# Kernel optimization log

Hardware: AMD Instinct MI355X
Metric: run time of the kernel (lower is better)

Reference implementation:

```python
import jax, jax.numpy as jnp
import numpy as np

T, K, N = 4096, 4096, 11008  # tokens, in_features, out_features


def _unpack_int4(packed):
    """packed: int8 [..., K//2] -> signed 4-bit values int8 [..., K].
    Low nibble first, high nibble second; arithmetic shifts sign-extend."""
    lo = jnp.right_shift(jnp.left_shift(packed, 4).astype(jnp.int8), 4)
    hi = jnp.right_shift(packed, 4).astype(jnp.int8)
    out = jnp.stack([lo, hi], axis=-1)  # [..., K//2, 2]
    return out.reshape(*packed.shape[:-1], packed.shape[-1] * 2)


def _pack_int4(vals):
    """vals: int8 in [-8,7], [..., K] -> packed int8 [..., K//2]."""
    v = vals.reshape(*vals.shape[:-1], vals.shape[-1] // 2, 2)
    lo = v[..., 0] & 0xF
    hi = v[..., 1] & 0xF
    return (lo | jnp.left_shift(hi, 4)).astype(jnp.int8)


def setup_inputs() -> dict:
    key = jax.random.key(0)
    k1, k2, k3, k4 = jax.random.split(key, 4)
    # symmetric 4-bit quantized values in [-7, 7], packed two per byte
    x_int = jax.random.randint(k1, (T, K), -7, 8).astype(jnp.int8)
    w_int = jax.random.randint(k2, (N, K), -7, 8).astype(jnp.int8)
    pq_x = _pack_int4(x_int)
    weight = _pack_int4(w_int)
    # per-token / per-output-channel dequant scales (max_abs/7 style magnitudes)
    scales_x = (jax.random.uniform(k3, (T,), jnp.float32) * 0.01 + 1e-4)
    weight_scales = (jax.random.uniform(k4, (N,), jnp.float32) * 0.01 + 1e-4)
    return {"pq_x": pq_x, "scales_x": scales_x, "weight": weight,
            "weight_scales": weight_scales}


def reference(pq_x, scales_x, weight, weight_scales):
    # Unpack int4 operands. Products |a*w| <= 49 and K=4096 => |acc| <= 2e5,
    # exactly representable in fp32, so the fp32 matmul equals int32 GEMM.
    a = _unpack_int4(pq_x).astype(jnp.float32)      # [T, K]
    w = _unpack_int4(weight).astype(jnp.float32)    # [N, K]
    acc = jnp.einsum('tk,nk->tn', a, w)             # integer GEMM in fp32
    # fused per-token x per-output-channel dequant
    out = acc * scales_x[:, None] * weight_scales[None, :]
    out = out.astype(jnp.float16)
    return out[None]  # unsqueeze(0) as in the torch module
```

## Files before the change

### kernel.cpp

```cpp
#include <hip/hip_runtime.h>
#include <hip/hip_fp16.h>
#include <stdint.h>


#define T_DIM 4096
#define K_DIM 4096
#define N_DIM 11008
#define KP    2048
#define BM 128
#define BN 128
#define BK 64
#define STAGES 64
#define A_PANELS (T_DIM / BM)
#define B_PANELS (N_DIM / BN)
#define CHUNK 8192
#define WS_A ((size_t)A_PANELS * STAGES * CHUNK)
#define WS_B ((size_t)B_PANELS * STAGES * CHUNK)
#define NA_BYTES ((size_t)T_DIM * KP)
#define NW_BYTES ((size_t)N_DIM * KP)

typedef __attribute__((ext_vector_type(4)))  int int32x4;
typedef __attribute__((ext_vector_type(16))) int int32x16;
typedef __attribute__((ext_vector_type(4)))  float floatx4;
typedef __attribute__((ext_vector_type(8)))  _Float16 f16x8;
typedef __attribute__((ext_vector_type(2)))  _Float16 f16x2;

__device__ __forceinline__ uint32_t pack4(int4 v) {
  return (uint32_t)(v.x & 0xFF) | ((uint32_t)(v.y & 0xFF) << 8) |
         ((uint32_t)(v.z & 0xFF) << 16) | ((uint32_t)(v.w & 0xFF) << 24);
}
__device__ __forceinline__ uint32_t nib_lo_s8(uint32_t p) {
  uint32_t t = (p & 0x0F0F0F0Fu) ^ 0x88888888u;
  return (t - 0x08080808u) ^ 0x80808080u;
}
__device__ __forceinline__ uint32_t nib_hi_s8(uint32_t p) {
  uint32_t t = ((p >> 4) & 0x0F0F0F0Fu) ^ 0x88888888u;
  return (t - 0x08080808u) ^ 0x80808080u;
}

__global__ __launch_bounds__(256) void unpack_tiles(
    const int* __restrict__ xa, const int* __restrict__ xw,
    uint8_t* __restrict__ wsa, uint8_t* __restrict__ wsb)
{
  const int row = blockIdx.x;
  const int g = threadIdx.x;
  const int s = g >> 2, c = g & 3;
  const int* src; uint8_t* dst; int r;
  if (row < T_DIM) {
    src = xa + (size_t)row * KP;
    r = row & (BM - 1);
    dst = wsa + ((size_t)((row >> 7) * STAGES + s)) * CHUNK;
  } else {
    const int rw = row - T_DIM;
    src = xw + (size_t)rw * KP;
    r = rw & (BN - 1);
    dst = wsb + ((size_t)((rw >> 7) * STAGES + s)) * CHUNK;
  }
  const int4* s4 = (const int4*)(src + g * 8);
  const int4 v0 = s4[0], v1 = s4[1];
  const uint32_t b0 = pack4(v0), b1 = pack4(v1);
  uint4 o;
  o.x = nib_lo_s8(b0); o.y = nib_hi_s8(b0);
  o.z = nib_lo_s8(b1); o.w = nib_hi_s8(b1);
  *(uint4*)(dst + c * 2048 + r * 16) = o;
}

__device__ __forceinline__ void dma16(const uint8_t* g, uint8_t* l) {
  __builtin_amdgcn_global_load_lds(
      (const __attribute__((address_space(1))) uint32_t*)g,
      (__attribute__((address_space(3))) uint32_t*)l, 16, 0, 0);
}

__global__ __launch_bounds__(256) void gemm_i8(
    const uint8_t* __restrict__ wsa, const uint8_t* __restrict__ wsb,
    const float* __restrict__ sx, const float* __restrict__ sw,
    float* __restrict__ out)
{
  __shared__ uint8_t sA[CHUNK];
  __shared__ uint8_t sB[CHUNK];

  const int tid  = threadIdx.x;
  const int lane = tid & 63;
  const int wv   = tid >> 6;
  const int wm   = wv >> 1, wn = wv & 1;
  const int h    = lane >> 5;
  const int ml   = lane & 31;
  const int p    = blockIdx.x;
  const int q    = blockIdx.y;

  const uint8_t* chunkA = wsa + (size_t)p * STAGES * CHUNK;
  const uint8_t* chunkB = wsb + (size_t)q * STAGES * CHUNK;
  const int seg = wv * 2048 + lane * 16;
  uint8_t* ldsA0 = &sA[wv * 2048];
  uint8_t* ldsB0 = &sB[wv * 2048];

  const int rowA = (wm * 64 + ml) * 16;
  const int rowB = (wn * 64 + ml) * 16;

  int32x16 acc00, acc01, acc10, acc11;
#pragma unroll
  for (int i = 0; i < 16; ++i) { acc00[i] = 0; acc01[i] = 0; acc10[i] = 0; acc11[i] = 0; }

  dma16(chunkA + seg, ldsA0);
  dma16(chunkA + seg + 1024, ldsA0 + 1024);
  dma16(chunkB + seg, ldsB0);
  dma16(chunkB + seg + 1024, ldsB0 + 1024);

#pragma unroll 1
  for (int s = 0; s < STAGES; ++s) {
    __syncthreads();
#pragma unroll
    for (int s2 = 0; s2 < 2; ++s2) {
      const uint8_t* pa = &sA[(2 * s2 + h) * 2048 + rowA];
      const uint8_t* pb = &sB[(2 * s2 + h) * 2048 + rowB];
      const int32x4 a0 = *(const int32x4*)pa;
      const int32x4 a1 = *(const int32x4*)(pa + 512);
      const int32x4 b0 = *(const int32x4*)pb;
      const int32x4 b1 = *(const int32x4*)(pb + 512);
      acc00 = __builtin_amdgcn_mfma_i32_32x32x32_i8(a0, b0, acc00, 0, 0, 0);
      acc01 = __builtin_amdgcn_mfma_i32_32x32x32_i8(a0, b1, acc01, 0, 0, 0);
      acc10 = __builtin_amdgcn_mfma_i32_32x32x32_i8(a1, b0, acc10, 0, 0, 0);
      acc11 = __builtin_amdgcn_mfma_i32_32x32x32_i8(a1, b1, acc11, 0, 0, 0);
    }
    __syncthreads();
    if (s + 1 < STAGES) {
      const uint8_t* ca = chunkA + (size_t)(s + 1) * CHUNK + seg;
      const uint8_t* cb = chunkB + (size_t)(s + 1) * CHUNK + seg;
      dma16(ca, ldsA0);
      dma16(ca + 1024, ldsA0 + 1024);
      dma16(cb, ldsB0);
      dma16(cb + 1024, ldsB0 + 1024);
    }
  }

#pragma unroll
  for (int mi = 0; mi < 2; ++mi) {
    const int rb = p * BM + wm * 64 + mi * 32 + 4 * h;
#pragma unroll
    for (int ni = 0; ni < 2; ++ni) {
      const int gcol = q * BN + wn * 64 + ni * 32 + ml;
      const float swv = sw[gcol];
      const int32x16 a = (mi == 0) ? (ni == 0 ? acc00 : acc01)
                                   : (ni == 0 ? acc10 : acc11);
#pragma unroll
      for (int r = 0; r < 16; ++r) {
        const int grow = rb + (r & 3) + 8 * (r >> 2);
        const float v = (float)a[r] * sx[grow] * swv;
        out[(size_t)grow * N_DIM + gcol] = __half2float(__float2half(v));
      }
    }
  }
}

__global__ __launch_bounds__(256) void repack_int32_to_bytes(
    const int* __restrict__ xa, const int* __restrict__ xw,
    uint32_t* __restrict__ da, uint32_t* __restrict__ dw)
{
  const size_t i = (size_t)blockIdx.x * blockDim.x + threadIdx.x;
  const size_t na4 = NA_BYTES / 4;
  const int4* src; uint32_t* dst; size_t off;
  if (i < na4) { src = (const int4*)xa; dst = da; off = i; }
  else         { src = (const int4*)xw; dst = dw; off = i - na4; }
  const int4 v = src[off];
  dst[off] = pack4(v);
}

__device__ __forceinline__ uint32_t cvt2(uint32_t m) {
  union U { uint32_t u; f16x2 h; } a, b, c;
  a.u = m ^ 0x64086408u; b.u = 0xE408E408u; c.h = a.h + b.h;
  return c.u;
}
__device__ __forceinline__ void unpack_cell(uint32_t* cell, uint32_t p) {
  cell[0] = cvt2( p        & 0x000F000Fu);
  cell[1] = cvt2((p >> 4)  & 0x000F000Fu);
  cell[2] = cvt2((p >> 8)  & 0x000F000Fu);
  cell[3] = cvt2((p >> 12) & 0x000F000Fu);
}

template <bool PACKED>
__global__ __launch_bounds__(256) void linear4bit_f16(
    const uint8_t* __restrict__ pqx, const float* __restrict__ sx,
    const uint8_t* __restrict__ wq,  const float* __restrict__ sw,
    const int* __restrict__ pqx32,   const int* __restrict__ wq32,
    float* __restrict__ out)
{
  __shared__ uint32_t sAf[8][BM][4];
  __shared__ uint32_t sBf[8][BN][4];
  const int tid = threadIdx.x, lane = tid & 63, wv = tid >> 6;
  const int wm = wv >> 1, wn = wv & 1, qd = lane >> 4, m16 = lane & 15;
  const int bm0 = blockIdx.x * BM, bn0 = blockIdx.y * BN;
  const int srow = tid >> 1, sh = tid & 1;
  const uint8_t* aPtr = pqx + (size_t)(bm0 + srow) * KP + sh * 16;
  const uint8_t* bPtr = wq  + (size_t)(bn0 + srow) * KP + sh * 16;
  const int* aPtr32 = pqx32 + (size_t)(bm0 + srow) * KP + sh * 16;
  const int* bPtr32 = wq32  + (size_t)(bn0 + srow) * KP + sh * 16;
  floatx4 acc[4][4];
#pragma unroll
  for (int mi = 0; mi < 4; ++mi)
#pragma unroll
    for (int ni = 0; ni < 4; ++ni)
#pragma unroll
      for (int r = 0; r < 4; ++r) acc[mi][ni][r] = 0.0f;
  uint4 ar, br;
  auto load_stage = [&](int s) {
    if (PACKED) {
      ar = *(const uint4*)(aPtr + (size_t)s * 32);
      br = *(const uint4*)(bPtr + (size_t)s * 32);
    } else {
      const int4* a4 = (const int4*)(aPtr32 + (size_t)s * 32);
      const int4* b4 = (const int4*)(bPtr32 + (size_t)s * 32);
      ar.x = pack4(a4[0]); ar.y = pack4(a4[1]); ar.z = pack4(a4[2]); ar.w = pack4(a4[3]);
      br.x = pack4(b4[0]); br.y = pack4(b4[1]); br.z = pack4(b4[2]); br.w = pack4(b4[3]);
    }
  };
  auto stage_to_lds = [&]() {
    uint32_t pa[4] = {ar.x, ar.y, ar.z, ar.w};
    uint32_t pb[4] = {br.x, br.y, br.z, br.w};
#pragma unroll
    for (int i = 0; i < 4; ++i) {
      unpack_cell(&sAf[4 * sh + i][srow][0], pa[i]);
      unpack_cell(&sBf[4 * sh + i][srow][0], pb[i]);
    }
  };
  load_stage(0); stage_to_lds();
#pragma unroll 1
  for (int s = 0; s < STAGES; ++s) {
    __syncthreads();
    if (s + 1 < STAGES) load_stage(s + 1);
#pragma unroll
    for (int s2 = 0; s2 < 2; ++s2) {
      f16x8 aF[4], bF[4];
#pragma unroll
      for (int mi = 0; mi < 4; ++mi)
        aF[mi] = *(const f16x8*)&sAf[4 * s2 + qd][wm * 64 + mi * 16 + m16][0];
#pragma unroll
      for (int ni = 0; ni < 4; ++ni)
        bF[ni] = *(const f16x8*)&sBf[4 * s2 + qd][wn * 64 + ni * 16 + m16][0];
#pragma unroll
      for (int mi = 0; mi < 4; ++mi)
#pragma unroll
        for (int ni = 0; ni < 4; ++ni)
          acc[mi][ni] = __builtin_amdgcn_mfma_f32_16x16x32_f16(aF[mi], bF[ni], acc[mi][ni], 0, 0, 0);
    }
    __syncthreads();
    if (s + 1 < STAGES) stage_to_lds();
  }
#pragma unroll
  for (int mi = 0; mi < 4; ++mi) {
    const int grow0 = bm0 + wm * 64 + mi * 16 + qd * 4;
    const float s0 = sx[grow0], s1 = sx[grow0 + 1], s2v = sx[grow0 + 2], s3 = sx[grow0 + 3];
#pragma unroll
    for (int ni = 0; ni < 4; ++ni) {
      const int gcol = bn0 + wn * 64 + ni * 16 + m16;
      const float swv = sw[gcol];
      const floatx4 a = acc[mi][ni];
      out[(size_t)(grow0 + 0) * N_DIM + gcol] = __half2float(__float2half(a[0] * s0 * swv));
      out[(size_t)(grow0 + 1) * N_DIM + gcol] = __half2float(__float2half(a[1] * s1 * swv));
      out[(size_t)(grow0 + 2) * N_DIM + gcol] = __half2float(__float2half(a[2] * s2v * swv));
      out[(size_t)(grow0 + 3) * N_DIM + gcol] = __half2float(__float2half(a[3] * s3 * swv));
    }
  }
}

extern "C" void kernel_launch(void* const* d_in, const int* in_sizes, int n_in,
                              void* d_out, int out_size, void* d_ws, size_t ws_size,
                              hipStream_t stream) {
  const int*   pqx32 = (const int*)d_in[0];
  const float* sxp   = (const float*)d_in[1];
  const int*   wq32  = (const int*)d_in[2];
  const float* swp   = (const float*)d_in[3];
  float* outp = (float*)d_out;

  if (ws_size >= WS_A + WS_B) {
    uint8_t* wsa = (uint8_t*)d_ws;
    uint8_t* wsb = wsa + WS_A;
    unpack_tiles<<<T_DIM + N_DIM, 256, 0, stream>>>(pqx32, wq32, wsa, wsb);
    gemm_i8<<<dim3(A_PANELS, B_PANELS), 256, 0, stream>>>(wsa, wsb, sxp, swp, outp);
  } else if (ws_size >= NA_BYTES + NW_BYTES) {
    uint8_t* da = (uint8_t*)d_ws;
    uint8_t* dw = da + NA_BYTES;
    const size_t total4 = (NA_BYTES + NW_BYTES) / 4;
    repack_int32_to_bytes<<<(uint32_t)(total4 / 256), 256, 0, stream>>>(
        pqx32, wq32, (uint32_t*)da, (uint32_t*)dw);
    linear4bit_f16<true><<<dim3(T_DIM / BM, N_DIM / BN), 256, 0, stream>>>(
        da, sxp, dw, swp, nullptr, nullptr, outp);
  } else {
    linear4bit_f16<false><<<dim3(T_DIM / BM, N_DIM / BN), 256, 0, stream>>>(
        nullptr, sxp, nullptr, swp, pqx32, wq32, outp);
  }
}
```

Before: 492.6 us.

## Widen int8 GEMM tile to 128x256 with double-buffered LDS prefetch

The N tile of the pre-unpacked int8 MFMA GEMM grows from 128 to 256, so each wave computes 2x4 32x32 MFMA tiles, raising reuse of each A fragment. LDS is double-buffered and the next stage's global-to-LDS DMA is issued right after a single barrier, overlapping it with the current stage's MFMAs. The unpack kernel is reorganised to write the new 256-row B chunk layout, and per-row activation scales are hoisted in the epilogue. The cost is more accumulator registers (128 VGPRs of accumulators) and 48KB of LDS per block, which may limit occupancy despite the launch-bounds hint.

```diff
diff --git a/kernel.cpp b/kernel.cpp
--- a/kernel.cpp
+++ b/kernel.cpp
@@ -8,14 +8,14 @@
 #define N_DIM 11008
 #define KP    2048
 #define BM 128
-#define BN 128
-#define BK 64
+#define BN 256
 #define STAGES 64
 #define A_PANELS (T_DIM / BM)
 #define B_PANELS (N_DIM / BN)
-#define CHUNK 8192
-#define WS_A ((size_t)A_PANELS * STAGES * CHUNK)
-#define WS_B ((size_t)B_PANELS * STAGES * CHUNK)
+#define CHUNK_A 8192
+#define CHUNK_B 16384
+#define WS_A ((size_t)A_PANELS * STAGES * CHUNK_A)
+#define WS_B ((size_t)B_PANELS * STAGES * CHUNK_B)
 #define NA_BYTES ((size_t)T_DIM * KP)
 #define NW_BYTES ((size_t)N_DIM * KP)
 
@@ -38,31 +38,39 @@
   return (t - 0x08080808u) ^ 0x80808080u;
 }
 
-__global__ __launch_bounds__(256) void unpack_tiles(
+__global__ __launch_bounds__(256) void unpack_tiles2(
     const int* __restrict__ xa, const int* __restrict__ xw,
     uint8_t* __restrict__ wsa, uint8_t* __restrict__ wsb)
 {
-  const int row = blockIdx.x;
-  const int g = threadIdx.x;
-  const int s = g >> 2, c = g & 3;
-  const int* src; uint8_t* dst; int r;
-  if (row < T_DIM) {
-    src = xa + (size_t)row * KP;
-    r = row & (BM - 1);
-    dst = wsa + ((size_t)((row >> 7) * STAGES + s)) * CHUNK;
+  const int s  = blockIdx.x;
+  const int yb = blockIdx.y;
+  const int t  = threadIdx.x;
+  const int r  = t >> 1, h = t & 1;
+
+  const int* src; uint8_t* dst; int cellStride;
+  if (yb < A_PANELS) {
+    src = xa + ((size_t)(yb * 128 + r)) * KP + s * 32 + h * 16;
+    dst = wsa + ((size_t)yb * STAGES + s) * CHUNK_A + r * 16;
+    cellStride = 2048;
   } else {
-    const int rw = row - T_DIM;
-    src = xw + (size_t)rw * KP;
-    r = rw & (BN - 1);
-    dst = wsb + ((size_t)((rw >> 7) * STAGES + s)) * CHUNK;
-  }
-  const int4* s4 = (const int4*)(src + g * 8);
-  const int4 v0 = s4[0], v1 = s4[1];
+    const int yb2 = yb - A_PANELS;
+    const int panel = yb2 >> 1;
+    const int rip = (yb2 & 1) * 128 + r;
+    src = xw + ((size_t)(yb2 * 128 + r)) * KP + s * 32 + h * 16;
+    dst = wsb + ((size_t)panel * STAGES + s) * CHUNK_B + rip * 16;
+    cellStride = 4096;
+  }
+  const int4* s4 = (const int4*)src;
+  const int4 v0 = s4[0], v1 = s4[1], v2 = s4[2], v3 = s4[3];
   const uint32_t b0 = pack4(v0), b1 = pack4(v1);
-  uint4 o;
-  o.x = nib_lo_s8(b0); o.y = nib_hi_s8(b0);
-  o.z = nib_lo_s8(b1); o.w = nib_hi_s8(b1);
-  *(uint4*)(dst + c * 2048 + r * 16) = o;
+  const uint32_t b2 = pack4(v2), b3 = pack4(v3);
+  uint4 o01, o23;
+  o01.x = nib_lo_s8(b0); o01.y = nib_hi_s8(b0);
+  o01.z = nib_lo_s8(b1); o01.w = nib_hi_s8(b1);
+  o23.x = nib_lo_s8(b2); o23.y = nib_hi_s8(b2);
+  o23.z = nib_lo_s8(b3); o23.w = nib_hi_s8(b3);
+  *(uint4*)(dst + (2 * h    ) * cellStride) = o01;
+  *(uint4*)(dst + (2 * h + 1) * cellStride) = o23;
 }
 
 __device__ __forceinline__ void dma16(const uint8_t* g, uint8_t* l) {
@@ -71,13 +79,13 @@
       (__attribute__((address_space(3))) uint32_t*)l, 16, 0, 0);
 }
 
-__global__ __launch_bounds__(256) void gemm_i8(
+__global__ __launch_bounds__(256, 2) void gemm_i8_db(
     const uint8_t* __restrict__ wsa, const uint8_t* __restrict__ wsb,
     const float* __restrict__ sx, const float* __restrict__ sw,
     float* __restrict__ out)
 {
-  __shared__ uint8_t sA[CHUNK];
-  __shared__ uint8_t sB[CHUNK];
+  __shared__ uint8_t sA[2][CHUNK_A];
+  __shared__ uint8_t sB[2][CHUNK_B];
 
   const int tid  = threadIdx.x;
   const int lane = tid & 63;
@@ -85,67 +93,76 @@
   const int wm   = wv >> 1, wn = wv & 1;
   const int h    = lane >> 5;
   const int ml   = lane & 31;
-  const int p    = blockIdx.x;
-  const int q    = blockIdx.y;
-
-  const uint8_t* chunkA = wsa + (size_t)p * STAGES * CHUNK;
-  const uint8_t* chunkB = wsb + (size_t)q * STAGES * CHUNK;
-  const int seg = wv * 2048 + lane * 16;
-  uint8_t* ldsA0 = &sA[wv * 2048];
-  uint8_t* ldsB0 = &sB[wv * 2048];
+  const int pp   = blockIdx.x;
+  const int qq   = blockIdx.y;
+
+  const uint8_t* chunkA = wsa + (size_t)pp * STAGES * CHUNK_A;
+  const uint8_t* chunkB = wsb + (size_t)qq * STAGES * CHUNK_B;
+  const int segOff = wv * 1024 + lane * 16;
+  const int ldsOff = wv * 1024;
 
   const int rowA = (wm * 64 + ml) * 16;
-  const int rowB = (wn * 64 + ml) * 16;
-
-  int32x16 acc00, acc01, acc10, acc11;
-#pragma unroll
-  for (int i = 0; i < 16; ++i) { acc00[i] = 0; acc01[i] = 0; acc10[i] = 0; acc11[i] = 0; }
-
-  dma16(chunkA + seg, ldsA0);
-  dma16(chunkA + seg + 1024, ldsA0 + 1024);
-  dma16(chunkB + seg, ldsB0);
-  dma16(chunkB + seg + 1024, ldsB0 + 1024);
+  const int rowB = (wn * 128 + ml) * 16;
+
+  int32x16 acc[2][4];
+#pragma unroll
+  for (int mi = 0; mi < 2; ++mi)
+#pragma unroll
+    for (int ni = 0; ni < 4; ++ni)
+#pragma unroll
+      for (int i = 0; i < 16; ++i) acc[mi][ni][i] = 0;
+
+  auto dma_stage = [&](int s, int buf) {
+    const uint8_t* ca = chunkA + (size_t)s * CHUNK_A;
+    const uint8_t* cb = chunkB + (size_t)s * CHUNK_B;
+#pragma unroll
+    for (int i = 0; i < 2; ++i)
+      dma16(ca + segOff + i * 4096, &sA[buf][ldsOff + i * 4096]);
+#pragma unroll
+    for (int i = 0; i < 4; ++i)
+      dma16(cb + segOff + i * 4096, &sB[buf][ldsOff + i * 4096]);
+  };
+
+  dma_stage(0, 0);
 
 #pragma unroll 1
   for (int s = 0; s < STAGES; ++s) {
+    const int buf = s & 1;
     __syncthreads();
+    if (s + 1 < STAGES) dma_stage(s + 1, buf ^ 1);
 #pragma unroll
     for (int s2 = 0; s2 < 2; ++s2) {
-      const uint8_t* pa = &sA[(2 * s2 + h) * 2048 + rowA];
-      const uint8_t* pb = &sB[(2 * s2 + h) * 2048 + rowB];
-      const int32x4 a0 = *(const int32x4*)pa;
-      const int32x4 a1 = *(const int32x4*)(pa + 512);
-      const int32x4 b0 = *(const int32x4*)pb;
-      const int32x4 b1 = *(const int32x4*)(pb + 512);
-      acc00 = __builtin_amdgcn_mfma_i32_32x32x32_i8(a0, b0, acc00, 0, 0, 0);
-      acc01 = __builtin_amdgcn_mfma_i32_32x32x32_i8(a0, b1, acc01, 0, 0, 0);
-      acc10 = __builtin_amdgcn_mfma_i32_32x32x32_i8(a1, b0, acc10, 0, 0, 0);
-      acc11 = __builtin_amdgcn_mfma_i32_32x32x32_i8(a1, b1, acc11, 0, 0, 0);
-    }
-    __syncthreads();
-    if (s + 1 < STAGES) {
-      const uint8_t* ca = chunkA + (size_t)(s + 1) * CHUNK + seg;
-      const uint8_t* cb = chunkB + (size_t)(s + 1) * CHUNK + seg;
-      dma16(ca, ldsA0);
-      dma16(ca + 1024, ldsA0 + 1024);
-      dma16(cb, ldsB0);
-      dma16(cb + 1024, ldsB0 + 1024);
+      const int c = 2 * s2 + h;
+      const uint8_t* pa = &sA[buf][c * 2048 + rowA];
+      const uint8_t* pb = &sB[buf][c * 4096 + rowB];
+      int32x4 aF[2], bF[4];
+#pragma unroll
+      for (int mi = 0; mi < 2; ++mi) aF[mi] = *(const int32x4*)(pa + mi * 512);
+#pragma unroll
+      for (int ni = 0; ni < 4; ++ni) bF[ni] = *(const int32x4*)(pb + ni * 512);
+#pragma unroll
+      for (int mi = 0; mi < 2; ++mi)
+#pragma unroll
+        for (int ni = 0; ni < 4; ++ni)
+          acc[mi][ni] = __builtin_amdgcn_mfma_i32_32x32x32_i8(
+              aF[mi], bF[ni], acc[mi][ni], 0, 0, 0);
     }
   }
 
 #pragma unroll
   for (int mi = 0; mi < 2; ++mi) {
-    const int rb = p * BM + wm * 64 + mi * 32 + 4 * h;
-#pragma unroll
-    for (int ni = 0; ni < 2; ++ni) {
-      const int gcol = q * BN + wn * 64 + ni * 32 + ml;
+    const int rb = pp * BM + wm * 64 + mi * 32 + 4 * h;
+    float sxv[16];
+#pragma unroll
+    for (int r = 0; r < 16; ++r) sxv[r] = sx[rb + (r & 3) + 8 * (r >> 2)];
+#pragma unroll
+    for (int ni = 0; ni < 4; ++ni) {
+      const int gcol = qq * BN + wn * 128 + ni * 32 + ml;
       const float swv = sw[gcol];
-      const int32x16 a = (mi == 0) ? (ni == 0 ? acc00 : acc01)
-                                   : (ni == 0 ? acc10 : acc11);
 #pragma unroll
       for (int r = 0; r < 16; ++r) {
         const int grow = rb + (r & 3) + 8 * (r >> 2);
-        const float v = (float)a[r] * sx[grow] * swv;
+        const float v = (float)acc[mi][ni][r] * sxv[r] * swv;
         out[(size_t)grow * N_DIM + gcol] = __half2float(__float2half(v));
       }
     }
@@ -184,11 +201,11 @@
     const int* __restrict__ pqx32,   const int* __restrict__ wq32,
     float* __restrict__ out)
 {
-  __shared__ uint32_t sAf[8][BM][4];
-  __shared__ uint32_t sBf[8][BN][4];
+  __shared__ uint32_t sAf[8][128][4];
+  __shared__ uint32_t sBf[8][128][4];
   const int tid = threadIdx.x, lane = tid & 63, wv = tid >> 6;
   const int wm = wv >> 1, wn = wv & 1, qd = lane >> 4, m16 = lane & 15;
-  const int bm0 = blockIdx.x * BM, bn0 = blockIdx.y * BN;
+  const int bm0 = blockIdx.x * 128, bn0 = blockIdx.y * 128;
   const int srow = tid >> 1, sh = tid & 1;
   const uint8_t* aPtr = pqx + (size_t)(bm0 + srow) * KP + sh * 16;
   const uint8_t* bPtr = wq  + (size_t)(bn0 + srow) * KP + sh * 16;
@@ -274,18 +291,19 @@
   if (ws_size >= WS_A + WS_B) {
     uint8_t* wsa = (uint8_t*)d_ws;
     uint8_t* wsb = wsa + WS_A;
-    unpack_tiles<<<T_DIM + N_DIM, 256, 0, stream>>>(pqx32, wq32, wsa, wsb);
-    gemm_i8<<<dim3(A_PANELS, B_PANELS), 256, 0, stream>>>(wsa, wsb, sxp, swp, outp);
+    unpack_tiles2<<<dim3(STAGES, A_PANELS + N_DIM / 128), 256, 0, stream>>>(
+        pqx32, wq32, wsa, wsb);
+    gemm_i8_db<<<dim3(A_PANELS, B_PANELS), 256, 0, stream>>>(wsa, wsb, sxp, swp, outp);
   } else if (ws_size >= NA_BYTES + NW_BYTES) {
     uint8_t* da = (uint8_t*)d_ws;
     uint8_t* dw = da + NA_BYTES;
     const size_t total4 = (NA_BYTES + NW_BYTES) / 4;
     repack_int32_to_bytes<<<(uint32_t)(total4 / 256), 256, 0, stream>>>(
         pqx32, wq32, (uint32_t*)da, (uint32_t*)dw);
-    linear4bit_f16<true><<<dim3(T_DIM / BM, N_DIM / BN), 256, 0, stream>>>(
+    linear4bit_f16<true><<<dim3(T_DIM / 128, N_DIM / 128), 256, 0, stream>>>(
         da, sxp, dw, swp, nullptr, nullptr, outp);
   } else {
-    linear4bit_f16<false><<<dim3(T_DIM / BM, N_DIM / BN), 256, 0, stream>>>(
+    linear4bit_f16<false><<<dim3(T_DIM / 128, N_DIM / 128), 256, 0, stream>>>(
         nullptr, sxp, nullptr, swp, pqx32, wq32, outp);
   }
 }
```

Measured after the change: 477.7 us. 1.03x faster.
